# Kernel optimization log

Hardware: AMD Instinct MI355X
Metric: run time of the kernel (lower is better)

Reference implementation:

```python
import jax, jax.numpy as jnp
import numpy as np
from jax import lax

T, B = 128, 256
I, H = 512, 1024
V, O = 128, 64


def setup_inputs() -> dict:
    key = jax.random.key(0)
    ks = jax.random.split(key, 8)
    s_ih = 1.0 / np.sqrt(H)
    return {
        "input": jax.random.randint(ks[0], (T, B), 0, V, dtype=jnp.int64),
        "h0": jnp.zeros((1, B, H), jnp.float32),
        "c0": jnp.zeros((1, B, H), jnp.float32),
        "emb": jax.random.normal(ks[1], (V, I), jnp.float32),
        "w_ih": jax.random.uniform(ks[2], (4 * H, I), jnp.float32, -s_ih, s_ih),
        "w_hh": jax.random.uniform(ks[3], (4 * H, H), jnp.float32, -s_ih, s_ih),
        "b_ih": jax.random.uniform(ks[4], (4 * H,), jnp.float32, -s_ih, s_ih),
        "b_hh": jax.random.uniform(ks[5], (4 * H,), jnp.float32, -s_ih, s_ih),
        "w_out": jax.random.uniform(ks[6], (O, H), jnp.float32, -s_ih, s_ih),
        "b_out": jax.random.uniform(ks[7], (O,), jnp.float32, -s_ih, s_ih),
    }


def reference(input, h0, c0, emb, w_ih, w_hh, b_ih, b_hh, w_out, b_out):
    # Embedding lookup: [T, B] -> [T, B, I]
    x = emb[input]
    b = b_ih + b_hh  # fuse the two bias adds

    def step(carry, xt):
        h, c = carry  # [B, H] each
        gates = xt @ w_ih.T + h @ w_hh.T + b  # [B, 4H]
        i, f, g, o = jnp.split(gates, 4, axis=-1)  # torch gate order: i,f,g,o
        i = jax.nn.sigmoid(i)
        f = jax.nn.sigmoid(f)
        g = jnp.tanh(g)
        o = jax.nn.sigmoid(o)
        c_new = f * c + i * g
        h_new = o * jnp.tanh(c_new)
        return (h_new, c_new), h_new

    (h_last, _), _ = lax.scan(step, (h0[0], c0[0]), x)
    # out_layer(lstm_out[-1].unsqueeze(0))[-1] == last hidden through linear head
    return h_last @ w_out.T + b_out  # [B, O]
```

## Files before the change

### kernel.cpp

```cpp
#include <hip/hip_runtime.h>

typedef __attribute__((ext_vector_type(4)))  int int4v;
typedef __attribute__((ext_vector_type(16))) int i32x16;

union B16 { int4v v; signed char c[16]; };

__device__ __forceinline__ float sigm(float x){ return 1.f / (1.f + __expf(-x)); }
__device__ __forceinline__ float tanh_(float x){
  float e = __expf(-2.f * fabsf(x));
  float r = (1.f - e) / (1.f + e);
  return copysignf(r, x);
}
__device__ __forceinline__ void h_limbs(float h, int& a1, int& a0){
  float f1 = floorf(h * 128.f);
  f1 = fminf(fmaxf(f1, -128.f), 127.f);
  float r = fmaf(h, 32768.f, f1 * -256.f) - 128.f;
  float f0 = fminf(rintf(r), 127.f);
  a1 = (int)f1; a0 = (int)f0;
}

__device__ __forceinline__ void issue_l128_cc(const void* p, int4v& d){
  asm volatile("global_load_dwordx4 %0, %1, off sc0 sc1" : "=&v"(d) : "v"(p) : "memory");
}

__global__ __launch_bounds__(256) void prep_kernel(
    const float* __restrict__ emb, const float* __restrict__ w_ih,
    const float* __restrict__ b_ih, const float* __restrict__ b_hh,
    const float* __restrict__ h0, float* __restrict__ G_in,
    char* __restrict__ a1buf, char* __restrict__ a0buf)
{
  __shared__ __align__(16) float wt[16 * 512];
  const int tid = threadIdx.x;
  const int colbase = blockIdx.x << 4;
  #pragma unroll
  for (int i = 0; i < 8; ++i){
    int f = tid + (i << 8);
    int r = f >> 7, q = (f & 127) << 2;
    *(float4*)&wt[(r << 9) + q] = *(const float4*)&w_ih[((size_t)(colbase + r) << 9) + q];
  }
  __syncthreads();
  const int v_ = tid & 127, ch = tid >> 7;
  float acc[8] = {0,0,0,0,0,0,0,0};
  const float* ep = emb + ((size_t)v_ << 9);
  for (int kq = 0; kq < 128; ++kq){
    float4 e = *(const float4*)(ep + (kq << 2));
    #pragma unroll
    for (int c = 0; c < 8; ++c){
      float4 w = *(const float4*)&wt[(((ch << 3) + c) << 9) + (kq << 2)];
      acc[c] += e.x * w.x + e.y * w.y + e.z * w.z + e.w * w.w;
    }
  }
  const int col0 = colbase + (ch << 3);
  #pragma unroll
  for (int c = 0; c < 8; ++c) acc[c] += b_ih[col0 + c] + b_hh[col0 + c];
  float* gp = &G_in[((size_t)v_ << 12) + col0];
  float4 r0 = {acc[0], acc[1], acc[2], acc[3]};
  float4 r1 = {acc[4], acc[5], acc[6], acc[7]};
  *(float4*)gp = r0;
  *(float4*)(gp + 4) = r1;

  int g0 = (blockIdx.x << 10) + (tid << 2);
  float4 hv = *(const float4*)&h0[g0];
  int a1x,a0x,a1y,a0y,a1z,a0z,a1w,a0w;
  h_limbs(hv.x, a1x, a0x); h_limbs(hv.y, a1y, a0y);
  h_limbs(hv.z, a1z, a0z); h_limbs(hv.w, a1w, a0w);
  unsigned u1 = (unsigned)(a1x & 255) | ((unsigned)(a1y & 255) << 8)
              | ((unsigned)(a1z & 255) << 16) | ((unsigned)(a1w & 255) << 24);
  unsigned u0 = (unsigned)(a0x & 255) | ((unsigned)(a0y & 255) << 8)
              | ((unsigned)(a0z & 255) << 16) | ((unsigned)(a0w & 255) << 24);
  ((unsigned*)a1buf)[g0 >> 2] = u1;
  ((unsigned*)a0buf)[g0 >> 2] = u0;
}

__global__ __launch_bounds__(256, 1) void lstm_kernel(
    const int* __restrict__ input, const float* __restrict__ c0,
    const float* __restrict__ w_hh, const float* __restrict__ w_out,
    const float* __restrict__ b_out, const float* __restrict__ G_in,
    char* __restrict__ a1base, char* __restrict__ a0base,
    unsigned* __restrict__ flags, float* __restrict__ out)
{
  const int tid  = threadIdx.x;
  const int lane = tid & 63;
  const int wid  = tid >> 6;
  const int bg   = blockIdx.x >> 5;
  const int cg   = blockIdx.x & 31;
  const int bl   = tid >> 3;
  const int u4   = (tid & 7) << 2;
  const int row  = tid & 31;
  const int grp  = tid >> 5;

  __shared__ __align__(16) unsigned long long sA1[4096];
  __shared__ __align__(16) unsigned long long sA0[4096];
  __shared__ __align__(16) float sG[32 * 132];
  __shared__ float sKc[128];

  int4v b1f[32], b0f[32];
  {
    const float* wrow = w_hh + (size_t)(wid * 1024 + cg * 32 + (lane & 31)) * 1024;
    const int kb0 = (lane >> 5) << 4;
    float csum = 0.f;
    #pragma unroll
    for (int ks = 0; ks < 32; ++ks){
      B16 v1, v0;
      #pragma unroll
      for (int q = 0; q < 4; ++q){
        float4 w4 = *(const float4*)&wrow[ks * 32 + kb0 + (q << 2)];
        float wa[4] = {w4.x, w4.y, w4.z, w4.w};
        #pragma unroll
        for (int j = 0; j < 4; ++j){
          float w = wa[j];
          csum += w;
          float s1 = rintf(w * 2048.f);
          float s0 = fminf(rintf(fmaf(w, 524288.f, s1 * -256.f)), 127.f);
          v1.c[(q << 2) + j] = (signed char)(int)s1;
          v0.c[(q << 2) + j] = (signed char)(int)s0;
        }
      }
      b1f[ks] = v1.v; b0f[ks] = v0.v;
    }
    csum += __shfl_xor(csum, 32, 64);
    if (lane < 32) sKc[(wid << 5) + lane] = csum * 0.00390625f;
  }

  const int b = (bg << 5) + bl;
  float4 cr = *(const float4*)&c0[((size_t)b << 10) + (cg << 5) + u4];
  unsigned* slots = &flags[bg * 32];
  unsigned* myslot = &flags[bg * 32 + cg];
  const size_t rbase = (size_t)((bg << 5) + row) << 10;

  #pragma unroll 1
  for (int t = 0; t < 128; ++t){
    const char* s1b = a1base + (size_t)(t & 1) * 262144;
    const char* s0b = a0base + (size_t)(t & 1) * 262144;
    char* d1b = a1base + (size_t)((t + 1) & 1) * 262144;
    char* d0b = a0base + (size_t)((t + 1) & 1) * 262144;
    const unsigned target = (unsigned)t;

    int iv = input[t * 256 + b];
    const float* gp = G_in + ((size_t)iv << 12) + (cg << 5) + u4;
    float4 q0 = *(const float4*)(gp);
    float4 q1 = *(const float4*)(gp + 1024);
    float4 q2 = *(const float4*)(gp + 2048);
    float4 q3 = *(const float4*)(gp + 3072);

    if (wid == 0 && target){
      int guard = 0;
      for (;;){
        unsigned v = (lane < 32)
          ? __hip_atomic_load(&slots[lane], __ATOMIC_RELAXED, __HIP_MEMORY_SCOPE_AGENT)
          : 0xFFFFFFFFu;
        if (__ballot(lane >= 16 || v >= target) == ~0ull) break;
        if (++guard > (1 << 20)) break;
      }
    }
    __syncthreads();

    int4v gv1[8], gv0[8];
    #pragma unroll
    for (int i = 0; i < 4; ++i){
      size_t off = rbase + ((size_t)(grp + (i << 3)) << 4);
      issue_l128_cc(s1b + off, gv1[i]);
      issue_l128_cc(s0b + off, gv0[i]);
    }

    if (wid == 0 && target){
      int guard = 0;
      for (;;){
        unsigned v = (lane < 32)
          ? __hip_atomic_load(&slots[lane], __ATOMIC_RELAXED, __HIP_MEMORY_SCOPE_AGENT)
          : 0xFFFFFFFFu;
        if (__ballot(v >= target) == ~0ull) break;
        if (++guard > (1 << 20)) break;
      }
    }
    __syncthreads();

    #pragma unroll
    for (int i = 4; i < 8; ++i){
      size_t off = rbase + ((size_t)(grp + (i << 3)) << 4);
      issue_l128_cc(s1b + off, gv1[i]);
      issue_l128_cc(s0b + off, gv0[i]);
    }
    asm volatile("s_waitcnt vmcnt(0)" ::: "memory");
    __builtin_amdgcn_sched_barrier(0);
    #pragma unroll
    for (int i = 0; i < 8; ++i){
      int m = grp + (i << 3);
      int lidx = ((((m >> 1) << 6) + ((m & 1) << 5) + row)) << 1;
      *(int4v*)&sA1[lidx] = gv1[i];
      *(int4v*)&sA0[lidx] = gv0[i];
    }
    __syncthreads();

    i32x16 acc_hi = {}, acc_m1 = {}, acc_m2 = {};
    const int4v* A1 = (const int4v*)sA1;
    const int4v* A0 = (const int4v*)sA0;
    #pragma unroll
    for (int ks = 0; ks < 32; ++ks){
      int4v af1 = A1[(ks << 6) + lane];
      acc_hi = __builtin_amdgcn_mfma_i32_32x32x32_i8(af1, b1f[ks], acc_hi, 0, 0, 0);
      acc_m1 = __builtin_amdgcn_mfma_i32_32x32x32_i8(af1, b0f[ks], acc_m1, 0, 0, 0);
      int4v af0 = A0[(ks << 6) + lane];
      acc_m2 = __builtin_amdgcn_mfma_i32_32x32x32_i8(af0, b1f[ks], acc_m2, 0, 0, 0);
    }

    {
      const int col = (wid << 5) + (lane & 31);
      const int rb  = (lane >> 5) << 2;
      #pragma unroll
      for (int r = 0; r < 16; ++r){
        int rrow = (r & 3) + ((r >> 2) << 3) + rb;
        sG[rrow * 132 + col] = 3.814697265625e-06f     * (float)acc_hi[r]
                             + 1.4901161193847656e-08f * (float)(acc_m1[r] + acc_m2[r]);
      }
    }
    __syncthreads();

    {
      float4 kI = *(const float4*)&sKc[ 0 + u4];
      float4 kF = *(const float4*)&sKc[32 + u4];
      float4 kG = *(const float4*)&sKc[64 + u4];
      float4 kO = *(const float4*)&sKc[96 + u4];
      float4 gI = *(const float4*)&sG[bl * 132 +  0 + u4];
      float4 gF = *(const float4*)&sG[bl * 132 + 32 + u4];
      float4 gG = *(const float4*)&sG[bl * 132 + 64 + u4];
      float4 gO = *(const float4*)&sG[bl * 132 + 96 + u4];
      int a1x,a0x,a1y,a0y,a1z,a0z,a1w,a0w;
      { float I=sigm(gI.x+q0.x+kI.x), F=sigm(gF.x+q1.x+kF.x), G=tanh_(gG.x+q2.x+kG.x), O=sigm(gO.x+q3.x+kO.x);
        float Cn=F*cr.x+I*G; cr.x=Cn; h_limbs(O*tanh_(Cn), a1x, a0x); }
      { float I=sigm(gI.y+q0.y+kI.y), F=sigm(gF.y+q1.y+kF.y), G=tanh_(gG.y+q2.y+kG.y), O=sigm(gO.y+q3.y+kO.y);
        float Cn=F*cr.y+I*G; cr.y=Cn; h_limbs(O*tanh_(Cn), a1y, a0y); }
      { float I=sigm(gI.z+q0.z+kI.z), F=sigm(gF.z+q1.z+kF.z), G=tanh_(gG.z+q2.z+kG.z), O=sigm(gO.z+q3.z+kO.z);
        float Cn=F*cr.z+I*G; cr.z=Cn; h_limbs(O*tanh_(Cn), a1z, a0z); }
      { float I=sigm(gI.w+q0.w+kI.w), F=sigm(gF.w+q1.w+kF.w), G=tanh_(gG.w+q2.w+kG.w), O=sigm(gO.w+q3.w+kO.w);
        float Cn=F*cr.w+I*G; cr.w=Cn; h_limbs(O*tanh_(Cn), a1w, a0w); }
      unsigned u1 = (unsigned)(a1x & 255) | ((unsigned)(a1y & 255) << 8)
                  | ((unsigned)(a1z & 255) << 16) | ((unsigned)(a1w & 255) << 24);
      unsigned u0 = (unsigned)(a0x & 255) | ((unsigned)(a0y & 255) << 8)
                  | ((unsigned)(a0z & 255) << 16) | ((unsigned)(a0w & 255) << 24);
      size_t eidx = (((size_t)b << 10) + (cg << 5) + u4) >> 2;
      __hip_atomic_store((unsigned*)d1b + eidx, u1, __ATOMIC_RELAXED, __HIP_MEMORY_SCOPE_AGENT);
      __hip_atomic_store((unsigned*)d0b + eidx, u0, __ATOMIC_RELAXED, __HIP_MEMORY_SCOPE_AGENT);
    }
    __syncthreads();
    if (tid == 0)
      __hip_atomic_store(myslot, (unsigned)(t + 1), __ATOMIC_RELAXED, __HIP_MEMORY_SCOPE_AGENT);
  }

  if (wid == 0){
    int guard = 0;
    for (;;){
      unsigned v = (lane < 32)
        ? __hip_atomic_load(&slots[lane], __ATOMIC_RELAXED, __HIP_MEMORY_SCOPE_AGENT)
        : 0xFFFFFFFFu;
      if (__ballot(v >= 128u) == ~0ull) break;
      if (++guard > (1 << 20)) break;
    }
  }
  __syncthreads();
  {
    const unsigned* h1p = (const unsigned*)a1base;
    const unsigned* h0p = (const unsigned*)a0base;
    const int ksl = tid & 7;
    const int o0 = cg << 1;
    float s0 = 0.f, s1 = 0.f;
    const float* w0p = w_out + ((size_t)o0 << 10);
    const float* w1p = w0p + 1024;
    for (int k = ksl * 128; k < ksl * 128 + 128; k += 4){
      size_t idx = (((size_t)b << 10) + k) >> 2;
      unsigned v1 = __hip_atomic_load(h1p + idx, __ATOMIC_RELAXED, __HIP_MEMORY_SCOPE_AGENT);
      unsigned v0 = __hip_atomic_load(h0p + idx, __ATOMIC_RELAXED, __HIP_MEMORY_SCOPE_AGENT);
      float4 w0 = *(const float4*)(w0p + k);
      float4 w1 = *(const float4*)(w1p + k);
      float hh[4];
      #pragma unroll
      for (int j = 0; j < 4; ++j){
        int A1j = (int)(signed char)((v1 >> (8 * j)) & 255);
        int A0j = (int)(signed char)((v0 >> (8 * j)) & 255);
        hh[j] = (float)(A1j * 256 + A0j + 128) * 3.0517578125e-05f;
      }
      s0 += hh[0]*w0.x + hh[1]*w0.y + hh[2]*w0.z + hh[3]*w0.w;
      s1 += hh[0]*w1.x + hh[1]*w1.y + hh[2]*w1.z + hh[3]*w1.w;
    }
    sG[bl * 16 + (ksl << 1)]     = s0;
    sG[bl * 16 + (ksl << 1) + 1] = s1;
  }
  __syncthreads();
  if (tid < 64){
    int bl2 = tid >> 1, ol = tid & 1;
    float s = b_out[(cg << 1) + ol];
    #pragma unroll
    for (int q = 0; q < 8; ++q) s += sG[bl2 * 16 + (q << 1) + ol];
    out[((size_t)((bg << 5) + bl2) << 6) + (cg << 1) + ol] = s;
  }
}

extern "C" void kernel_launch(void* const* d_in, const int* in_sizes, int n_in,
                              void* d_out, int out_size, void* d_ws, size_t ws_size,
                              hipStream_t stream){
  (void)in_sizes; (void)n_in; (void)out_size; (void)ws_size;
  const int* input   = (const int*)d_in[0];
  const float* h0    = (const float*)d_in[1];
  const float* c0    = (const float*)d_in[2];
  const float* emb   = (const float*)d_in[3];
  const float* w_ih  = (const float*)d_in[4];
  const float* w_hh  = (const float*)d_in[5];
  const float* b_ih  = (const float*)d_in[6];
  const float* b_hh  = (const float*)d_in[7];
  const float* w_out = (const float*)d_in[8];
  const float* b_out = (const float*)d_in[9];
  float* out = (float*)d_out;

  char* ws = (char*)d_ws;
  float* G_in   = (float*)ws;
  char* a1buf   = ws + (2u << 20);
  char* a0buf   = ws + (2u << 20) + (512u << 10);
  unsigned* flags = (unsigned*)(ws + (3u << 20));

  hipMemsetAsync(flags, 0, 4096, stream);
  prep_kernel<<<dim3(256), dim3(256), 0, stream>>>(emb, w_ih, b_ih, b_hh, h0, G_in, a1buf, a0buf);

  void* args[] = {(void*)&input, (void*)&c0, (void*)&w_hh, (void*)&w_out, (void*)&b_out,
                  (void*)&G_in, (void*)&a1buf, (void*)&a0buf, (void*)&flags, (void*)&out};
  if (hipLaunchCooperativeKernel((void*)lstm_kernel, dim3(256), dim3(256), args, 0, stream)
      != hipSuccess){
    lstm_kernel<<<dim3(256), dim3(256), 0, stream>>>(input, c0, w_hh, w_out, b_out,
                                                     G_in, a1buf, a0buf, flags, out);
  }
}
```

Baseline: 1.095 ms.

## Pipeline h-limb loads with MFMA in four chunks after a single full wait

The two-phase wait (first half of producer slots, then all) becomes a single wait for all producers before any loads are issued. The loads are then consumed in four chunks with graded vmcnt waits and workgroup barriers, so LDS staging and MFMA on earlier k-chunks overlap the remaining global loads. This trades the earlier overlap of the first-half loads with the second wait for overlap of load latency with compute, and adds three extra s_barriers per step.

```diff
diff --git a/kernel.cpp b/kernel.cpp
--- a/kernel.cpp
+++ b/kernel.cpp
@@ -149,59 +149,53 @@
         unsigned v = (lane < 32)
           ? __hip_atomic_load(&slots[lane], __ATOMIC_RELAXED, __HIP_MEMORY_SCOPE_AGENT)
           : 0xFFFFFFFFu;
-        if (__ballot(lane >= 16 || v >= target) == ~0ull) break;
+        if (__ballot(v >= target) == ~0ull) break;
         if (++guard > (1 << 20)) break;
       }
     }
     __syncthreads();
 
+    asm volatile("s_waitcnt vmcnt(0)" ::: "memory");
+    __builtin_amdgcn_sched_barrier(0);
+
     int4v gv1[8], gv0[8];
     #pragma unroll
-    for (int i = 0; i < 4; ++i){
+    for (int i = 0; i < 8; ++i){
       size_t off = rbase + ((size_t)(grp + (i << 3)) << 4);
       issue_l128_cc(s1b + off, gv1[i]);
       issue_l128_cc(s0b + off, gv0[i]);
     }
 
-    if (wid == 0 && target){
-      int guard = 0;
-      for (;;){
-        unsigned v = (lane < 32)
-          ? __hip_atomic_load(&slots[lane], __ATOMIC_RELAXED, __HIP_MEMORY_SCOPE_AGENT)
-          : 0xFFFFFFFFu;
-        if (__ballot(v >= target) == ~0ull) break;
-        if (++guard > (1 << 20)) break;
-      }
-    }
-    __syncthreads();
-
-    #pragma unroll
-    for (int i = 4; i < 8; ++i){
-      size_t off = rbase + ((size_t)(grp + (i << 3)) << 4);
-      issue_l128_cc(s1b + off, gv1[i]);
-      issue_l128_cc(s0b + off, gv0[i]);
-    }
-    asm volatile("s_waitcnt vmcnt(0)" ::: "memory");
-    __builtin_amdgcn_sched_barrier(0);
-    #pragma unroll
-    for (int i = 0; i < 8; ++i){
-      int m = grp + (i << 3);
-      int lidx = ((((m >> 1) << 6) + ((m & 1) << 5) + row)) << 1;
-      *(int4v*)&sA1[lidx] = gv1[i];
-      *(int4v*)&sA0[lidx] = gv0[i];
-    }
-    __syncthreads();
-
     i32x16 acc_hi = {}, acc_m1 = {}, acc_m2 = {};
     const int4v* A1 = (const int4v*)sA1;
     const int4v* A0 = (const int4v*)sA0;
     #pragma unroll
-    for (int ks = 0; ks < 32; ++ks){
-      int4v af1 = A1[(ks << 6) + lane];
-      acc_hi = __builtin_amdgcn_mfma_i32_32x32x32_i8(af1, b1f[ks], acc_hi, 0, 0, 0);
-      acc_m1 = __builtin_amdgcn_mfma_i32_32x32x32_i8(af1, b0f[ks], acc_m1, 0, 0, 0);
-      int4v af0 = A0[(ks << 6) + lane];
-      acc_m2 = __builtin_amdgcn_mfma_i32_32x32x32_i8(af0, b1f[ks], acc_m2, 0, 0, 0);
+    for (int c = 0; c < 4; ++c){
+      if      (c == 0) asm volatile("s_waitcnt vmcnt(12)" ::: "memory");
+      else if (c == 1) asm volatile("s_waitcnt vmcnt(8)"  ::: "memory");
+      else if (c == 2) asm volatile("s_waitcnt vmcnt(4)"  ::: "memory");
+      else             asm volatile("s_waitcnt vmcnt(0)"  ::: "memory");
+      __builtin_amdgcn_sched_barrier(0);
+      #pragma unroll
+      for (int j = 0; j < 2; ++j){
+        const int i = 2*c + j;
+        const int m = grp + (i << 3);
+        const int lidx = ((((m >> 1) << 6) + ((m & 1) << 5) + row)) << 1;
+        *(int4v*)&sA1[lidx] = gv1[i];
+        *(int4v*)&sA0[lidx] = gv0[i];
+      }
+      asm volatile("s_waitcnt lgkmcnt(0)" ::: "memory");
+      __builtin_amdgcn_sched_barrier(0);
+      __builtin_amdgcn_s_barrier();
+      __builtin_amdgcn_sched_barrier(0);
+      #pragma unroll
+      for (int ks = 8*c; ks < 8*c + 8; ++ks){
+        int4v af1 = A1[(ks << 6) + lane];
+        acc_hi = __builtin_amdgcn_mfma_i32_32x32x32_i8(af1, b1f[ks], acc_hi, 0, 0, 0);
+        acc_m1 = __builtin_amdgcn_mfma_i32_32x32x32_i8(af1, b0f[ks], acc_m1, 0, 0, 0);
+        int4v af0 = A0[(ks << 6) + lane];
+        acc_m2 = __builtin_amdgcn_mfma_i32_32x32x32_i8(af0, b1f[ks], acc_m2, 0, 0, 0);
+      }
     }
 
     {
```

Measured after the change: 1.039 ms. -5.1%, faster.
